# Performance work log

Hardware: AMD Instinct MI355X
Metric: run time of the kernel (lower is better)

## Reference

```python
import jax, jax.numpy as jnp
import numpy as np

D_MODEL = 1024
N_HEAD = 16
D_K = D_MODEL // N_HEAD


def setup_inputs() -> dict:
    key = jax.random.key(0)
    ks = jax.random.split(key, 12)
    B, S = 2, 2048
    s = 1.0 / np.sqrt(D_MODEL)
    return {
        "query": jax.random.normal(ks[0], (B, S, D_MODEL), jnp.float32),
        "key": jax.random.normal(ks[1], (B, S, D_MODEL), jnp.float32),
        "value": jax.random.normal(ks[2], (B, S, D_MODEL), jnp.float32),
        "Wq": jax.random.normal(ks[3], (D_MODEL, D_MODEL), jnp.float32) * s,
        "bq": jnp.zeros((D_MODEL,), jnp.float32),
        "Wk": jax.random.normal(ks[4], (D_MODEL, D_MODEL), jnp.float32) * s,
        "bk": jnp.zeros((D_MODEL,), jnp.float32),
        "Wv": jax.random.normal(ks[5], (D_MODEL, D_MODEL), jnp.float32) * s,
        "bv": jnp.zeros((D_MODEL,), jnp.float32),
        "Wo": jax.random.normal(ks[6], (D_MODEL, D_MODEL), jnp.float32) * s,
        "bo": jnp.zeros((D_MODEL,), jnp.float32),
    }


def reference(query, key, value, Wq, bq, Wk, bk, Wv, bv, Wo, bo):
    B, S, _ = query.shape
    # QKV projections (torch Linear: x @ W.T + b)
    q = query @ Wq.T + bq
    k = key @ Wk.T + bk
    v = value @ Wv.T + bv
    # [B, S, H, Dk] -> [B, H, S, Dk]
    q = q.reshape(B, S, N_HEAD, D_K).transpose(0, 2, 1, 3)
    k = k.reshape(B, -1, N_HEAD, D_K).transpose(0, 2, 1, 3)
    v = v.reshape(B, -1, N_HEAD, D_K).transpose(0, 2, 1, 3)
    # scores [B, H, Sq, Sk]
    attn = jnp.einsum("bhqd,bhkd->bhqk", q, k) / jnp.sqrt(jnp.float32(D_K))
    attn = jax.nn.softmax(attn, axis=-1)  # dropout p=0 -> identity
    out = jnp.einsum("bhqk,bhkd->bhqd", attn, v)
    out = out.transpose(0, 2, 1, 3).reshape(B, S, D_MODEL)
    return out @ Wo.T + bo
```

## Files before the change

kernel.cpp:

```cpp
#include <hip/hip_runtime.h>
#include <cstdint>
#include <cstddef>

#define DM 1024
#define NHEAD 16
#define DKH 64
#define SEQLEN 2048
#define NBATCH 2
#define MTOT (NBATCH * SEQLEN)

typedef __attribute__((ext_vector_type(8))) short bf16x8;
typedef __attribute__((ext_vector_type(4))) float f32x4;
typedef __attribute__((ext_vector_type(16))) float f32x16;
typedef __attribute__((ext_vector_type(2))) unsigned int u32x2;

#define QSCALE 0.18033688011112042f

__device__ __forceinline__ uint16_t f2bf(float f) {
  uint32_t x = __float_as_uint(f);
  uint32_t r = x + 0x7FFFu + ((x >> 16) & 1u);
  return (uint16_t)(r >> 16);
}

__device__ __forceinline__ uint32_t cvtpk(float a, float b) {
  uint32_t r;
  asm("v_cvt_pk_bf16_f32 %0, %1, %2" : "=v"(r) : "v"(a), "v"(b));
  return r;
}

__device__ __forceinline__ float exp2_fast(float x) {
  float r;
  asm("v_exp_f32 %0, %1" : "=v"(r) : "v"(x));
  return r;
}

__device__ __forceinline__ float max3f(float a, float b, float c) {
  float r;
  asm("v_max3_f32 %0, %1, %2, %3" : "=v"(r) : "v"(a), "v"(b), "v"(c));
  return r;
}

__device__ __forceinline__ void gload_lds16(const void* g, void* l) {
  __builtin_amdgcn_global_load_lds(
      (const __attribute__((address_space(1))) void*)g,
      (__attribute__((address_space(3))) void*)l, 16, 0, 0);
}

__device__ __forceinline__ int fsw(int r) { return ((r + (r >> 3)) & 7) << 4; }

struct CvtArgs {
  const float* src[7];
  uint16_t* dst[7];
  int end4[7];
};

__global__ void cvt_all_kernel(CvtArgs a) {
  int i = blockIdx.x * blockDim.x + threadIdx.x;
  int r = 0;
#pragma unroll
  for (int j = 0; j < 7; ++j)
    if (i >= a.end4[j]) r = j + 1;
  if (r >= 7) return;
  int local = i - (r == 0 ? 0 : a.end4[r - 1]);
  float4 v = reinterpret_cast<const float4*>(a.src[r])[local];
  uint64_t p = (uint64_t)f2bf(v.x) | ((uint64_t)f2bf(v.y) << 16) |
               ((uint64_t)f2bf(v.z) << 32) | ((uint64_t)f2bf(v.w) << 48);
  reinterpret_cast<uint64_t*>(a.dst[r])[local] = p;
}

__device__ __forceinline__ void qkv_stage(const uint16_t* __restrict__ A,
                                          const uint16_t* __restrict__ Bt,
                                          int brow, int bcol, int k0,
                                          uint16_t* smem, int buf, int wave, int lane) {
#pragma unroll
  for (int t = 0; t < 4; ++t) {
    const int c = wave * 4 + t;
    const int o = c * 1024 + lane * 16;
    const uint16_t* g;
    if (c < 8) {
      const int row = o >> 6, kk = (o & 63) >> 1;
      g = A + (size_t)(brow + row) * DM + (k0 + kk);
    } else {
      const int o2 = o - 8192;
      const int row = o2 >> 6, kk = (o2 & 63) >> 1;
      g = Bt + (size_t)(bcol + row) * DM + (k0 + kk);
    }
    gload_lds16(g, (char*)smem + buf * 16384 + c * 1024);
  }
}

__global__ __launch_bounds__(256)
void gemm_qkv(const uint16_t* __restrict__ xq, const uint16_t* __restrict__ xk,
              const uint16_t* __restrict__ xv, const uint16_t* __restrict__ wqkv,
              const float* __restrict__ bqp, const float* __restrict__ bkp,
              const float* __restrict__ bvp, uint16_t* __restrict__ Qp,
              uint16_t* __restrict__ Kp, uint16_t* __restrict__ VTp) {
  __shared__ uint16_t smem[2 * 8192];
  const int tid = threadIdx.x;
  const int wave = tid >> 6, lane = tid & 63;
  const int l15 = lane & 15, l4 = lane >> 4;
  const int proj = blockIdx.y >> 3;
  const int brow = blockIdx.x * 128, bcol = (blockIdx.y & 7) * 128;
  const int wr = (wave >> 1) * 64, wc = (wave & 1) * 64;
  const uint16_t* A = proj == 0 ? xq : proj == 1 ? xk : xv;
  const uint16_t* Bt = wqkv + (size_t)proj * DM * DM;
  const float* bias = proj == 0 ? bqp : proj == 1 ? bkp : bvp;

  const f32x4 fzero = {0.f, 0.f, 0.f, 0.f};
  f32x4 acc[4][4];
#pragma unroll
  for (int m = 0; m < 4; ++m)
#pragma unroll
    for (int n = 0; n < 4; ++n) acc[m][n] = fzero;

  qkv_stage(A, Bt, brow, bcol, 0, smem, 0, wave, lane);
  int cur = 0;
  for (int k0 = 0; k0 < DM; k0 += 32) {
    __syncthreads();
    if (k0 + 32 < DM)
      qkv_stage(A, Bt, brow, bcol, k0 + 32, smem, cur ^ 1, wave, lane);
    const uint16_t* At = smem + cur * 8192;
    const uint16_t* Bs = At + 4096;
    bf16x8 a[4], b[4];
#pragma unroll
    for (int m = 0; m < 4; ++m)
      a[m] = *(const bf16x8*)(At + (wr + m * 16 + l15) * 32 + l4 * 8);
#pragma unroll
    for (int n = 0; n < 4; ++n)
      b[n] = *(const bf16x8*)(Bs + (wc + n * 16 + l15) * 32 + l4 * 8);
#pragma unroll
    for (int m = 0; m < 4; ++m)
#pragma unroll
      for (int n = 0; n < 4; ++n)
        acc[m][n] = __builtin_amdgcn_mfma_f32_16x16x32_bf16(a[m], b[n], acc[m][n], 0, 0, 0);
    cur ^= 1;
  }

  const float scale = proj == 0 ? QSCALE : 1.0f;
  uint16_t* dstQK = proj == 0 ? Qp : Kp;
#pragma unroll
  for (int m = 0; m < 4; ++m) {
#pragma unroll
    for (int n = 0; n < 4; ++n) {
      const int gcol = bcol + wc + n * 16 + l15;
      const float bv = bias[gcol];
      if (proj == 2) {
        const int grow0 = brow + wr + m * 16 + l4 * 4;
        const int b_ = grow0 >> 11, s_ = grow0 & 2047;
        const int h_ = gcol >> 6, d_ = gcol & 63;
        uint16_t* dst = VTp + ((size_t)((b_ * NHEAD + h_) * DKH + d_)) * SEQLEN + s_;
        uint64_t pk = (uint64_t)f2bf(acc[m][n][0] + bv) |
                      ((uint64_t)f2bf(acc[m][n][1] + bv) << 16) |
                      ((uint64_t)f2bf(acc[m][n][2] + bv) << 32) |
                      ((uint64_t)f2bf(acc[m][n][3] + bv) << 48);
        *(uint64_t*)dst = pk;
      } else {
#pragma unroll
        for (int r = 0; r < 4; ++r) {
          const int grow = brow + wr + m * 16 + l4 * 4 + r;
          dstQK[(size_t)grow * DM + gcol] = f2bf((acc[m][n][r] + bv) * scale);
        }
      }
    }
  }
}

__device__ __forceinline__ void gemm_stage(const uint16_t* __restrict__ A,
                                           const uint16_t* __restrict__ Bt,
                                           int brow, int bcol, int k0,
                                           char* smem, int buf, int wave, int lane) {
#pragma unroll
  for (int t = 0; t < 8; ++t) {
    const int o = t * 4096 + wave * 1024 + lane * 16;
    const uint16_t* g;
    if (t < 4) {
      const int row = o >> 7, kk = (o & 127) >> 1;
      g = A + (size_t)(brow + row) * DM + (k0 + kk);
    } else {
      const int o2 = o - 16384;
      const int row = o2 >> 7, kk = (o2 & 127) >> 1;
      g = Bt + (size_t)(bcol + row) * DM + (k0 + kk);
    }
    gload_lds16(g, smem + buf * 32768 + t * 4096 + wave * 1024);
  }
}

__global__ __launch_bounds__(256)
void gemm_out(const uint16_t* __restrict__ A, const uint16_t* __restrict__ Bt,
              const float* __restrict__ bias, float* __restrict__ C) {
  __shared__ uint16_t smem[2 * 2 * 128 * 64];
  const int tid = threadIdx.x;
  const int wave = tid >> 6, lane = tid & 63;
  const int l15 = lane & 15, l4 = lane >> 4;
  const int brow = blockIdx.x * 128, bcol = blockIdx.y * 128;
  const int wr = (wave >> 1) * 64, wc = (wave & 1) * 64;

  const f32x4 fzero = {0.f, 0.f, 0.f, 0.f};
  f32x4 acc[4][4];
#pragma unroll
  for (int m = 0; m < 4; ++m)
#pragma unroll
    for (int n = 0; n < 4; ++n) acc[m][n] = fzero;

  gemm_stage(A, Bt, brow, bcol, 0, (char*)smem, 0, wave, lane);
  int cur = 0;
  for (int k0 = 0; k0 < DM; k0 += 64) {
    __syncthreads();
    if (k0 + 64 < DM)
      gemm_stage(A, Bt, brow, bcol, k0 + 64, (char*)smem, cur ^ 1, wave, lane);
    const uint16_t* At = smem + cur * 16384;
    const uint16_t* Bs = At + 8192;
#pragma unroll
    for (int ks = 0; ks < 2; ++ks) {
      bf16x8 a[4], b[4];
#pragma unroll
      for (int m = 0; m < 4; ++m)
        a[m] = *(const bf16x8*)(At + (wr + m * 16 + l15) * 64 + ks * 32 + l4 * 8);
#pragma unroll
      for (int n = 0; n < 4; ++n)
        b[n] = *(const bf16x8*)(Bs + (wc + n * 16 + l15) * 64 + ks * 32 + l4 * 8);
#pragma unroll
      for (int m = 0; m < 4; ++m)
#pragma unroll
        for (int n = 0; n < 4; ++n)
          acc[m][n] = __builtin_amdgcn_mfma_f32_16x16x32_bf16(a[m], b[n], acc[m][n], 0, 0, 0);
    }
    cur ^= 1;
  }

#pragma unroll
  for (int m = 0; m < 4; ++m) {
#pragma unroll
    for (int n = 0; n < 4; ++n) {
      const int gcol = bcol + wc + n * 16 + l15;
      const float bv = bias[gcol];
#pragma unroll
      for (int r = 0; r < 4; ++r) {
        const int grow = brow + wr + m * 16 + l4 * 4 + r;
        C[(size_t)grow * DM + gcol] = acc[m][n][r] + bv;
      }
    }
  }
}

__device__ __forceinline__ void stage_kv(const uint16_t* __restrict__ Kg,
                                         const uint16_t* __restrict__ Vg,
                                         char* buf, int wq, int lane) {
#pragma unroll
  for (int i = 0; i < 2; ++i) {
    const int base = i * 4096 + wq * 1024;
    const int row = i * 32 + wq * 8 + (lane >> 3);
    const int esw = (((lane & 7) << 4) ^ fsw(row)) >> 1;
    gload_lds16(Kg + (size_t)row * DM + esw, buf + base);
    gload_lds16(Vg + (size_t)row * SEQLEN + esw, buf + 8192 + base);
  }
}

__global__ __launch_bounds__(512)
void attn_fwd_kernel(const uint16_t* __restrict__ Qp, const uint16_t* __restrict__ Kp,
                     const uint16_t* __restrict__ VTp, uint16_t* __restrict__ Op) {
  __shared__ __align__(16) char lds[65536];
  const int swz = (blockIdx.x & 7) * 64 + (blockIdx.x >> 3);
  const int bb = swz >> 8, h = (swz >> 4) & 15;
  const int q0 = (swz & 15) * 128;
  const int tid = threadIdx.x;
  const int wave = tid >> 6, lane = tid & 63;
  const int wq = wave & 3, kh = wave >> 2;
  const int l31 = lane & 31, hi = lane >> 5;

  const int qrow = q0 + wq * 32 + l31;
  const uint16_t* qb = Qp + ((size_t)(bb * SEQLEN + qrow)) * DM + h * DKH;
  bf16x8 qf[4];
#pragma unroll
  for (int ds = 0; ds < 4; ++ds)
    qf[ds] = *(const bf16x8*)(qb + ds * 16 + hi * 8);

  bf16x8 onesf;
#pragma unroll
  for (int j = 0; j < 8; ++j) onesf[j] = (short)0x3F80;

  f32x16 oacc[2], lacc, zero16;
#pragma unroll
  for (int r = 0; r < 16; ++r) {
    oacc[0][r] = 0.f; oacc[1][r] = 0.f; lacc[r] = 0.f; zero16[r] = 0.f;
  }
  float mrow = -1e30f;

  const uint16_t* Kg = Kp + ((size_t)(bb * SEQLEN + kh * 1024)) * DM + h * DKH;
  const uint16_t* Vg = VTp + ((size_t)((bb * NHEAD + h) * DKH)) * SEQLEN + kh * 1024;
  char* my = lds + kh * 32768;

  stage_kv(Kg, Vg, my, wq, lane);

  const int NT = 1024 / 64;
  for (int t = 0; t < NT; ++t) {
    __syncthreads();
    if (t + 1 < NT)
      stage_kv(Kg + (size_t)(t + 1) * 64 * DM, Vg + (t + 1) * 64,
               my + ((t + 1) & 1) * 16384, wq, lane);
    const char* kb = my + (t & 1) * 16384;
    const char* vb = kb + 8192;

    f32x16 sacc[2];
    __builtin_amdgcn_s_setprio(1);
#pragma unroll
    for (int n = 0; n < 2; ++n) {
      const int kr = 32 * n + l31;
      const char* krow = kb + kr * 128;
      const int f = fsw(kr);
      const bf16x8 kf0 = *(const bf16x8*)(krow + ((hi * 16) ^ f));
      sacc[n] = __builtin_amdgcn_mfma_f32_32x32x16_bf16(kf0, qf[0], zero16, 0, 0, 0);
#pragma unroll
      for (int ds = 1; ds < 4; ++ds) {
        const bf16x8 kf = *(const bf16x8*)(krow + ((ds * 32 + hi * 16) ^ f));
        sacc[n] = __builtin_amdgcn_mfma_f32_32x32x16_bf16(kf, qf[ds], sacc[n], 0, 0, 0);
      }
    }
    __builtin_amdgcn_s_setprio(0);

    float ma = max3f(sacc[0][0], sacc[0][1], sacc[0][2]);
    ma = max3f(ma, sacc[0][3], sacc[0][4]);
    ma = max3f(ma, sacc[0][5], sacc[0][6]);
    ma = max3f(ma, sacc[0][7], sacc[0][8]);
    ma = max3f(ma, sacc[0][9], sacc[0][10]);
    ma = max3f(ma, sacc[0][11], sacc[0][12]);
    ma = max3f(ma, sacc[0][13], sacc[0][14]);
    float mb = max3f(sacc[1][0], sacc[1][1], sacc[1][2]);
    mb = max3f(mb, sacc[1][3], sacc[1][4]);
    mb = max3f(mb, sacc[1][5], sacc[1][6]);
    mb = max3f(mb, sacc[1][7], sacc[1][8]);
    mb = max3f(mb, sacc[1][9], sacc[1][10]);
    mb = max3f(mb, sacc[1][11], sacc[1][12]);
    mb = max3f(mb, sacc[1][13], sacc[1][14]);
    float mx = max3f(fmaxf(ma, sacc[0][15]), mb, sacc[1][15]);
    mx = fmaxf(mx, __shfl_xor(mx, 32, 64));

    float mnew = mrow;
    if (__any(mx > mrow + 8.f)) {
      mnew = fmaxf(mrow, mx);
      const float scl = exp2_fast(mrow - mnew);
#pragma unroll
      for (int m = 0; m < 2; ++m)
#pragma unroll
        for (int r = 0; r < 16; ++r) oacc[m][r] *= scl;
      lacc[0] *= scl;
    }
    mrow = mnew;

#pragma unroll
    for (int n = 0; n < 2; ++n) {
      float pv[16];
#pragma unroll
      for (int r = 0; r < 16; ++r) pv[r] = exp2_fast(sacc[n][r] - mnew);
      const uint32_t c0 = cvtpk(pv[0], pv[1]),   c1 = cvtpk(pv[2], pv[3]);
      const uint32_t c2 = cvtpk(pv[4], pv[5]),   c3 = cvtpk(pv[6], pv[7]);
      const uint32_t c4 = cvtpk(pv[8], pv[9]),   c5 = cvtpk(pv[10], pv[11]);
      const uint32_t c6 = cvtpk(pv[12], pv[13]), c7 = cvtpk(pv[14], pv[15]);
      const u32x2 r02 = __builtin_amdgcn_permlane32_swap(c0, c2, false, false);
      const u32x2 r13 = __builtin_amdgcn_permlane32_swap(c1, c3, false, false);
      const u32x2 r46 = __builtin_amdgcn_permlane32_swap(c4, c6, false, false);
      const u32x2 r57 = __builtin_amdgcn_permlane32_swap(c5, c7, false, false);
      union { uint32_t w[4]; bf16x8 v; } f0, f1;
      f0.w[0] = r02.x; f0.w[1] = r13.x; f0.w[2] = r02.y; f0.w[3] = r13.y;
      f1.w[0] = r46.x; f1.w[1] = r57.x; f1.w[2] = r46.y; f1.w[3] = r57.y;

      __builtin_amdgcn_s_setprio(1);
#pragma unroll
      for (int m = 0; m < 2; ++m) {
        const int vr = 32 * m + l31;
        const char* vrow = vb + vr * 128;
        const int f = fsw(vr);
        const bf16x8 v0 = *(const bf16x8*)(vrow + ((n * 64 + hi * 16) ^ f));
        const bf16x8 v1 = *(const bf16x8*)(vrow + ((n * 64 + 32 + hi * 16) ^ f));
        oacc[m] = __builtin_amdgcn_mfma_f32_32x32x16_bf16(v0, f0.v, oacc[m], 0, 0, 0);
        oacc[m] = __builtin_amdgcn_mfma_f32_32x32x16_bf16(v1, f1.v, oacc[m], 0, 0, 0);
      }
      lacc = __builtin_amdgcn_mfma_f32_32x32x16_bf16(onesf, f0.v, lacc, 0, 0, 0);
      lacc = __builtin_amdgcn_mfma_f32_32x32x16_bf16(onesf, f1.v, lacc, 0, 0, 0);
      __builtin_amdgcn_s_setprio(0);
    }
  }

  __syncthreads();
  char* mbuf = lds + wq * 16384 + lane * 144;
  if (kh == 1) {
    *(f32x16*)(mbuf) = oacc[0];
    *(f32x16*)(mbuf + 64) = oacc[1];
    *(float*)(mbuf + 128) = mrow;
    *(float*)(mbuf + 132) = lacc[0];
  }
  __syncthreads();
  if (kh == 1) return;

  const f32x16 o2a = *(const f32x16*)(mbuf);
  const f32x16 o2b = *(const f32x16*)(mbuf + 64);
  const float m2 = *(const float*)(mbuf + 128);
  const float l2 = *(const float*)(mbuf + 132);
  const float mstar = fmaxf(mrow, m2);
  const float a1 = exp2_fast(mrow - mstar);
  const float a2 = exp2_fast(m2 - mstar);
  const float il = 1.0f / (a1 * lacc[0] + a2 * l2);
  const float w1 = a1 * il, w2 = a2 * il;

  uint16_t* ob = Op + ((size_t)(bb * SEQLEN + qrow)) * DM + h * DKH;
#pragma unroll
  for (int m = 0; m < 2; ++m) {
    const f32x16 o2 = (m == 0) ? o2a : o2b;
#pragma unroll
    for (int rq = 0; rq < 4; ++rq) {
      const uint32_t w0 = cvtpk(oacc[m][4 * rq + 0] * w1 + o2[4 * rq + 0] * w2,
                                oacc[m][4 * rq + 1] * w1 + o2[4 * rq + 1] * w2);
      const uint32_t wA = cvtpk(oacc[m][4 * rq + 2] * w1 + o2[4 * rq + 2] * w2,
                                oacc[m][4 * rq + 3] * w1 + o2[4 * rq + 3] * w2);
      *(uint64_t*)(ob + 32 * m + 8 * rq + 4 * hi) =
          (uint64_t)w0 | ((uint64_t)wA << 32);
    }
  }
}

extern "C" void kernel_launch(void* const* d_in, const int* in_sizes, int n_in,
                              void* d_out, int out_size, void* d_ws, size_t ws_size,
                              hipStream_t stream) {
  (void)in_sizes; (void)n_in; (void)out_size; (void)ws_size;
  const float* query = (const float*)d_in[0];
  const float* key_i = (const float*)d_in[1];
  const float* value = (const float*)d_in[2];
  const float* Wq = (const float*)d_in[3];
  const float* bq = (const float*)d_in[4];
  const float* Wk = (const float*)d_in[5];
  const float* bk = (const float*)d_in[6];
  const float* Wv = (const float*)d_in[7];
  const float* bv = (const float*)d_in[8];
  const float* Wo = (const float*)d_in[9];
  const float* bo = (const float*)d_in[10];
  float* out = (float*)d_out;

  char* ws = (char*)d_ws;
  const size_t MB = 1ull << 20;
  uint16_t* xq  = (uint16_t*)(ws + 0 * MB);
  uint16_t* xk  = (uint16_t*)(ws + 8 * MB);
  uint16_t* xv  = (uint16_t*)(ws + 16 * MB);
  uint16_t* wqkv = (uint16_t*)(ws + 24 * MB);
  uint16_t* wob = (uint16_t*)(ws + 30 * MB);
  uint16_t* Qp  = (uint16_t*)(ws + 32 * MB);
  uint16_t* Kp  = (uint16_t*)(ws + 40 * MB);
  uint16_t* VTp = (uint16_t*)(ws + 48 * MB);
  uint16_t* AO  = (uint16_t*)(ws + 56 * MB);

  const int n4x = (MTOT * DM) / 4;
  const int n4w = (DM * DM) / 4;
  CvtArgs ca;
  ca.src[0] = query; ca.dst[0] = xq;
  ca.src[1] = key_i; ca.dst[1] = xk;
  ca.src[2] = value; ca.dst[2] = xv;
  ca.src[3] = Wq;    ca.dst[3] = wqkv;
  ca.src[4] = Wk;    ca.dst[4] = wqkv + DM * DM;
  ca.src[5] = Wv;    ca.dst[5] = wqkv + 2 * DM * DM;
  ca.src[6] = Wo;    ca.dst[6] = wob;
  int acc = 0;
  for (int j = 0; j < 7; ++j) { acc += (j < 3) ? n4x : n4w; ca.end4[j] = acc; }
  const int blk = 256;
  cvt_all_kernel<<<(acc + blk - 1) / blk, blk, 0, stream>>>(ca);

  dim3 gq(MTOT / 128, 24);
  gemm_qkv<<<gq, 256, 0, stream>>>(xq, xk, xv, wqkv, bq, bk, bv, Qp, Kp, VTp);

  attn_fwd_kernel<<<512, 512, 0, stream>>>(Qp, Kp, VTp, AO);

  dim3 gg(MTOT / 128, DM / 128);
  gemm_out<<<gg, 256, 0, stream>>>(AO, wob, bo, out);
}
```

Baseline: 125.9 us.

## Fuse fp32-to-bf16 activation conversion into QKV GEMM tile loads

Removes the separate conversion pass for the query/key/value activations. The QKV GEMM now loads fp32 rows into registers one tile ahead, converts them to bf16 after the MFMA step and stores them to shared memory; weights still stream via direct-to-LDS loads. This removes a full write and reread of the bf16 activations, but each tile now reads twice as many bytes of A, and the conversion adds VALU work inside the main loop.

```diff
diff --git a/kernel.cpp b/kernel.cpp
--- a/kernel.cpp
+++ b/kernel.cpp
@@ -49,18 +49,18 @@
 __device__ __forceinline__ int fsw(int r) { return ((r + (r >> 3)) & 7) << 4; }
 
 struct CvtArgs {
-  const float* src[7];
-  uint16_t* dst[7];
-  int end4[7];
+  const float* src[4];
+  uint16_t* dst[4];
+  int end4[4];
 };
 
 __global__ void cvt_all_kernel(CvtArgs a) {
   int i = blockIdx.x * blockDim.x + threadIdx.x;
   int r = 0;
 #pragma unroll
-  for (int j = 0; j < 7; ++j)
+  for (int j = 0; j < 4; ++j)
     if (i >= a.end4[j]) r = j + 1;
-  if (r >= 7) return;
+  if (r >= 4) return;
   int local = i - (r == 0 ? 0 : a.end4[r - 1]);
   float4 v = reinterpret_cast<const float4*>(a.src[r])[local];
   uint64_t p = (uint64_t)f2bf(v.x) | ((uint64_t)f2bf(v.y) << 16) |
@@ -68,30 +68,9 @@
   reinterpret_cast<uint64_t*>(a.dst[r])[local] = p;
 }
 
-__device__ __forceinline__ void qkv_stage(const uint16_t* __restrict__ A,
-                                          const uint16_t* __restrict__ Bt,
-                                          int brow, int bcol, int k0,
-                                          uint16_t* smem, int buf, int wave, int lane) {
-#pragma unroll
-  for (int t = 0; t < 4; ++t) {
-    const int c = wave * 4 + t;
-    const int o = c * 1024 + lane * 16;
-    const uint16_t* g;
-    if (c < 8) {
-      const int row = o >> 6, kk = (o & 63) >> 1;
-      g = A + (size_t)(brow + row) * DM + (k0 + kk);
-    } else {
-      const int o2 = o - 8192;
-      const int row = o2 >> 6, kk = (o2 & 63) >> 1;
-      g = Bt + (size_t)(bcol + row) * DM + (k0 + kk);
-    }
-    gload_lds16(g, (char*)smem + buf * 16384 + c * 1024);
-  }
-}
-
 __global__ __launch_bounds__(256)
-void gemm_qkv(const uint16_t* __restrict__ xq, const uint16_t* __restrict__ xk,
-              const uint16_t* __restrict__ xv, const uint16_t* __restrict__ wqkv,
+void gemm_qkv(const float* __restrict__ xq, const float* __restrict__ xk,
+              const float* __restrict__ xv, const uint16_t* __restrict__ wqkv,
               const float* __restrict__ bqp, const float* __restrict__ bkp,
               const float* __restrict__ bvp, uint16_t* __restrict__ Qp,
               uint16_t* __restrict__ Kp, uint16_t* __restrict__ VTp) {
@@ -102,10 +81,14 @@
   const int proj = blockIdx.y >> 3;
   const int brow = blockIdx.x * 128, bcol = (blockIdx.y & 7) * 128;
   const int wr = (wave >> 1) * 64, wc = (wave & 1) * 64;
-  const uint16_t* A = proj == 0 ? xq : proj == 1 ? xk : xv;
+  const float* A = proj == 0 ? xq : proj == 1 ? xk : xv;
   const uint16_t* Bt = wqkv + (size_t)proj * DM * DM;
   const float* bias = proj == 0 ? bqp : proj == 1 ? bkp : bvp;
 
+  const int ca = tid, cb = tid + 256;
+  const float* arow_a = A + (size_t)(brow + (ca >> 2)) * DM + (ca & 3) * 8;
+  const float* arow_b = A + (size_t)(brow + (cb >> 2)) * DM + (cb & 3) * 8;
+
   const f32x4 fzero = {0.f, 0.f, 0.f, 0.f};
   f32x4 acc[4][4];
 #pragma unroll
@@ -113,12 +96,48 @@
 #pragma unroll
     for (int n = 0; n < 4; ++n) acc[m][n] = fzero;
 
-  qkv_stage(A, Bt, brow, bcol, 0, smem, 0, wave, lane);
+  float4 p0, p1, p2, p3;
+  p0 = *(const float4*)(arow_a);
+  p1 = *(const float4*)(arow_a + 4);
+  p2 = *(const float4*)(arow_b);
+  p3 = *(const float4*)(arow_b + 4);
+#pragma unroll
+  for (int t = 0; t < 2; ++t) {
+    const int c = wave * 2 + t;
+    const int o = c * 1024 + lane * 16;
+    const int row = o >> 6, kk = (o & 63) >> 1;
+    gload_lds16(Bt + (size_t)(bcol + row) * DM + kk,
+                (char*)smem + 8192 + c * 1024);
+  }
+  {
+    uint4 w0, w1;
+    w0.x = cvtpk(p0.x, p0.y); w0.y = cvtpk(p0.z, p0.w);
+    w0.z = cvtpk(p1.x, p1.y); w0.w = cvtpk(p1.z, p1.w);
+    w1.x = cvtpk(p2.x, p2.y); w1.y = cvtpk(p2.z, p2.w);
+    w1.z = cvtpk(p3.x, p3.y); w1.w = cvtpk(p3.z, p3.w);
+    *(uint4*)((char*)smem + ca * 16) = w0;
+    *(uint4*)((char*)smem + cb * 16) = w1;
+  }
+
   int cur = 0;
   for (int k0 = 0; k0 < DM; k0 += 32) {
     __syncthreads();
-    if (k0 + 32 < DM)
-      qkv_stage(A, Bt, brow, bcol, k0 + 32, smem, cur ^ 1, wave, lane);
+    const bool hasNext = (k0 + 32 < DM);
+    if (hasNext) {
+      p0 = *(const float4*)(arow_a + k0 + 32);
+      p1 = *(const float4*)(arow_a + k0 + 36);
+      p2 = *(const float4*)(arow_b + k0 + 32);
+      p3 = *(const float4*)(arow_b + k0 + 36);
+#pragma unroll
+      for (int t = 0; t < 2; ++t) {
+        const int c = wave * 2 + t;
+        const int o = c * 1024 + lane * 16;
+        const int row = o >> 6, kk = (o & 63) >> 1;
+        gload_lds16(Bt + (size_t)(bcol + row) * DM + (k0 + 32 + kk),
+                    (char*)smem + (cur ^ 1) * 16384 + 8192 + c * 1024);
+      }
+    }
+
     const uint16_t* At = smem + cur * 8192;
     const uint16_t* Bs = At + 4096;
     bf16x8 a[4], b[4];
@@ -133,6 +152,16 @@
 #pragma unroll
       for (int n = 0; n < 4; ++n)
         acc[m][n] = __builtin_amdgcn_mfma_f32_16x16x32_bf16(a[m], b[n], acc[m][n], 0, 0, 0);
+
+    if (hasNext) {
+      uint4 w0, w1;
+      w0.x = cvtpk(p0.x, p0.y); w0.y = cvtpk(p0.z, p0.w);
+      w0.z = cvtpk(p1.x, p1.y); w0.w = cvtpk(p1.z, p1.w);
+      w1.x = cvtpk(p2.x, p2.y); w1.y = cvtpk(p2.z, p2.w);
+      w1.z = cvtpk(p3.x, p3.y); w1.w = cvtpk(p3.z, p3.w);
+      *(uint4*)((char*)smem + (cur ^ 1) * 16384 + ca * 16) = w0;
+      *(uint4*)((char*)smem + (cur ^ 1) * 16384 + cb * 16) = w1;
+    }
     cur ^= 1;
   }
 
@@ -437,9 +466,6 @@
 
   char* ws = (char*)d_ws;
   const size_t MB = 1ull << 20;
-  uint16_t* xq  = (uint16_t*)(ws + 0 * MB);
-  uint16_t* xk  = (uint16_t*)(ws + 8 * MB);
-  uint16_t* xv  = (uint16_t*)(ws + 16 * MB);
   uint16_t* wqkv = (uint16_t*)(ws + 24 * MB);
   uint16_t* wob = (uint16_t*)(ws + 30 * MB);
   uint16_t* Qp  = (uint16_t*)(ws + 32 * MB);
@@ -447,23 +473,19 @@
   uint16_t* VTp = (uint16_t*)(ws + 48 * MB);
   uint16_t* AO  = (uint16_t*)(ws + 56 * MB);
 
-  const int n4x = (MTOT * DM) / 4;
   const int n4w = (DM * DM) / 4;
   CvtArgs ca;
-  ca.src[0] = query; ca.dst[0] = xq;
-  ca.src[1] = key_i; ca.dst[1] = xk;
-  ca.src[2] = value; ca.dst[2] = xv;
-  ca.src[3] = Wq;    ca.dst[3] = wqkv;
-  ca.src[4] = Wk;    ca.dst[4] = wqkv + DM * DM;
-  ca.src[5] = Wv;    ca.dst[5] = wqkv + 2 * DM * DM;
-  ca.src[6] = Wo;    ca.dst[6] = wob;
+  ca.src[0] = Wq; ca.dst[0] = wqkv;
+  ca.src[1] = Wk; ca.dst[1] = wqkv + DM * DM;
+  ca.src[2] = Wv; ca.dst[2] = wqkv + 2 * DM * DM;
+  ca.src[3] = Wo; ca.dst[3] = wob;
   int acc = 0;
-  for (int j = 0; j < 7; ++j) { acc += (j < 3) ? n4x : n4w; ca.end4[j] = acc; }
+  for (int j = 0; j < 4; ++j) { acc += n4w; ca.end4[j] = acc; }
   const int blk = 256;
   cvt_all_kernel<<<(acc + blk - 1) / blk, blk, 0, stream>>>(ca);
 
   dim3 gq(MTOT / 128, 24);
-  gemm_qkv<<<gq, 256, 0, stream>>>(xq, xk, xv, wqkv, bq, bk, bv, Qp, Kp, VTp);
+  gemm_qkv<<<gq, 256, 0, stream>>>(query, key_i, value, wqkv, bq, bk, bv, Qp, Kp, VTp);
 
   attn_fwd_kernel<<<512, 512, 0, stream>>>(Qp, Kp, VTp, AO);
 
```

After: 141.0 us. 12.0% more time.
